# Kernel optimization log

Measured on AMD Instinct MI355X. Metric: run time of the kernel, lower is better.

## Reference

```python
import jax, jax.numpy as jnp
import numpy as np

B, T, C = 4, 2048, 1024
N_HEAD = 16
HEAD_DIM = C // N_HEAD


def setup_inputs() -> dict:
    key = jax.random.key(0)
    kx, kk, kq, kv, kp = jax.random.split(key, 5)
    s = 1.0 / np.sqrt(C)
    return {
        "x": jax.random.normal(kx, (B, T, C), dtype=jnp.float32),
        "Wk": jax.random.normal(kk, (C, C), dtype=jnp.float32) * s,
        "Wq": jax.random.normal(kq, (C, C), dtype=jnp.float32) * s,
        "Wv": jax.random.normal(kv, (C, C), dtype=jnp.float32) * s,
        "Wp": jax.random.normal(kp, (C, C), dtype=jnp.float32) * s,
    }


def reference(x, Wk, Wq, Wv, Wp):
    b, t, c = x.shape
    # torch nn.Linear(y = x @ W.T); split heads -> [B, H, T, D]
    def heads(w):
        return jnp.einsum("btc,ec->bte", x, w).reshape(b, t, N_HEAD, HEAD_DIM).transpose(0, 2, 1, 3)
    k = heads(Wk)
    q = heads(Wq)
    v = heads(Wv)
    scale = 1.0 / np.sqrt(HEAD_DIM).astype(np.float32)
    att = jnp.einsum("bhqd,bhkd->bhqk", q, k) * scale  # [B,H,T,T]
    causal = jnp.tril(jnp.ones((t, t), dtype=bool))
    att = jnp.where(causal[None, None], att, -jnp.inf)
    att = jax.nn.softmax(att, axis=-1)
    y = jnp.einsum("bhqk,bhkd->bhqd", att, v)  # [B,H,T,D]
    y = y.transpose(0, 2, 1, 3).reshape(b, t, c)
    return jnp.einsum("btc,ec->bte", y, Wp)
```

## Files before the change

### kernel.cpp

```cpp
#include <hip/hip_runtime.h>

typedef __bf16 bf16x8 __attribute__((ext_vector_type(8)));
typedef float f32x4 __attribute__((ext_vector_type(4)));
typedef float f32x16 __attribute__((ext_vector_type(16)));
typedef unsigned short u16x8 __attribute__((ext_vector_type(8)));
typedef unsigned short u16x4 __attribute__((ext_vector_type(4)));
typedef unsigned u32x4 __attribute__((ext_vector_type(4)));

#define BB 4
#define TT 2048
#define CC 1024
#define HH 16
#define DD 64

__device__ __forceinline__ unsigned short f2bf(float f){
  unsigned u = __builtin_bit_cast(unsigned, f);
  u += 0x7FFFu + ((u >> 16) & 1u);
  return (unsigned short)(u >> 16);
}
__device__ __forceinline__ bf16x8 as_bf(u16x8 v){ return __builtin_bit_cast(bf16x8, v); }
__device__ __forceinline__ unsigned cvt_pk(float lo, float hi){
  unsigned r; asm("v_cvt_pk_bf16_f32 %0, %1, %2" : "=v"(r) : "v"(lo), "v"(hi)); return r;
}
__device__ __forceinline__ void pl32swap(unsigned &a, unsigned &b){
  asm("v_permlane32_swap_b32 %0, %1" : "+v"(a), "+v"(b));
}
__device__ __forceinline__ float ex2(float x){
#if __has_builtin(__builtin_amdgcn_exp2f)
  return __builtin_amdgcn_exp2f(x);
#else
  return __expf(x * 0.6931471805599453f);
#endif
}

__global__ __launch_bounds__(256) void cvt_all(const float* __restrict__ x,
                                               const float* __restrict__ Wk,
                                               const float* __restrict__ Wq,
                                               const float* __restrict__ Wv,
                                               const float* __restrict__ Wp,
                                               unsigned short* __restrict__ xb,
                                               unsigned short* __restrict__ wb){
  const int i = blockIdx.x * 256 + threadIdx.x;
  constexpr int EX = (BB*TT*CC)/4;
  const float* src; unsigned short* dst; int off;
  if (i < EX){ src = x; dst = xb; off = i; }
  else {
    const int j = i - EX;
    const int wsel = j >> 18;
    off = j & 262143;
    src = (wsel==0) ? Wk : (wsel==1) ? Wq : (wsel==2) ? Wv : Wp;
    dst = wb + ((size_t)wsel << 20);
  }
  const float4 f = ((const float4*)src)[off];
  u16x4 o; o.x = f2bf(f.x); o.y = f2bf(f.y); o.z = f2bf(f.z); o.w = f2bf(f.w);
  ((u16x4*)dst)[off] = o;
}

template<int NX, bool QKV>
__global__ __launch_bounds__(256) void gemm128(const unsigned short* __restrict__ A,
                                               const unsigned short* __restrict__ Bm,
                                               void* __restrict__ o0, void* __restrict__ o1,
                                               void* __restrict__ o2){
  constexpr int K = 1024;
  constexpr int NWG = NX * 64;
  __shared__ __align__(16) unsigned short As[128*64];
  __shared__ __align__(16) unsigned short Bs[128*64];
  const int tid = threadIdx.x;
  const int flat = blockIdx.y * NX + blockIdx.x;
  const int swz = (flat & 7) * (NWG / 8) + (flat >> 3);
  const int n0 = (swz % NX) * 128;
  const int m0 = (swz / NX) * 128;
  const int w = tid >> 6, lane = tid & 63, l15 = lane & 15, g = lane >> 4;
  const int wm = (w >> 1) * 64, wn = (w & 1) * 64;

  f32x4 acc[4][4] = {};

  for (int k0 = 0; k0 < K; k0 += 64){
    #pragma unroll
    for (int i = 0; i < 4; ++i){
      const int p = i*256 + tid;
      const int r = p >> 3, c = p & 7;
      const int gc = c ^ (r & 7);
      __builtin_amdgcn_global_load_lds(
        (const __attribute__((address_space(1))) void*)(A + (size_t)(m0 + r)*K + k0 + gc*8),
        (__attribute__((address_space(3))) void*)(As + p*8), 16, 0, 0);
    }
    #pragma unroll
    for (int i = 0; i < 4; ++i){
      const int p = i*256 + tid;
      const int r = p >> 3, c = p & 7;
      const int gc = c ^ (r & 7);
      __builtin_amdgcn_global_load_lds(
        (const __attribute__((address_space(1))) void*)(Bm + (size_t)(n0 + r)*K + k0 + gc*8),
        (__attribute__((address_space(3))) void*)(Bs + p*8), 16, 0, 0);
    }
    __syncthreads();

    bf16x8 af[2][4], bfr[2][4];
    #pragma unroll
    for (int ks = 0; ks < 2; ++ks){
      #pragma unroll
      for (int m = 0; m < 4; ++m){
        const int R = wm + m*16 + l15;
        const int c = (ks*4 + g) ^ (R & 7);
        af[ks][m] = as_bf(*(const u16x8*)(As + R*64 + c*8));
      }
      #pragma unroll
      for (int n = 0; n < 4; ++n){
        const int R = wn + n*16 + l15;
        const int c = (ks*4 + g) ^ (R & 7);
        bfr[ks][n] = as_bf(*(const u16x8*)(Bs + R*64 + c*8));
      }
    }
    #pragma unroll
    for (int ks = 0; ks < 2; ++ks)
      #pragma unroll
      for (int m = 0; m < 4; ++m)
        #pragma unroll
        for (int n = 0; n < 4; ++n)
          acc[m][n] = __builtin_amdgcn_mfma_f32_16x16x32_bf16(af[ks][m], bfr[ks][n], acc[m][n], 0, 0, 0);
    __syncthreads();
  }

  const int tsel = n0 >> 10;
  const float sc = (QKV && tsel == 1) ? 0.18033688011112042f : 1.0f;
  unsigned short* outb = nullptr;
  if (QKV) outb = (unsigned short*)(tsel == 0 ? o0 : tsel == 1 ? o1 : o2);

  #pragma unroll
  for (int m = 0; m < 4; ++m)
    #pragma unroll
    for (int n = 0; n < 4; ++n)
      #pragma unroll
      for (int r = 0; r < 4; ++r){
        const int row = m0 + wm + m*16 + g*4 + r;
        const int col = n0 + wn + n*16 + l15;
        const float v = acc[m][n][r];
        if (QKV) outb[(size_t)row*1024 + (col & 1023)] = f2bf(v * sc);
        else     ((float*)o0)[(size_t)row*1024 + col] = v;
      }
}

__global__ __launch_bounds__(256) void transpose_v(const unsigned short* __restrict__ V,
                                                   unsigned short* __restrict__ Vt){
  __shared__ unsigned short Ts[64*72];
  const int kt = blockIdx.x, bh = blockIdx.y;
  const int b = bh >> 4, h = bh & 15;
  const int tid = threadIdx.x;
  #pragma unroll
  for (int i = 0; i < 2; ++i){
    const int p = i*256 + tid, r = p >> 3, c = p & 7;
    *(u16x8*)(Ts + r*72 + c*8) =
      *(const u16x8*)(V + (size_t)b*TT*CC + (size_t)(kt*64 + r)*CC + h*DD + c*8);
  }
  __syncthreads();
  #pragma unroll
  for (int i = 0; i < 2; ++i){
    const int p = i*256 + tid, d = p >> 3, c = p & 7;
    u16x8 v;
    #pragma unroll
    for (int j = 0; j < 8; ++j) v[j] = Ts[(c*8 + j)*72 + d];
    *(u16x8*)(Vt + ((size_t)bh*DD + d)*TT + (size_t)kt*64 + ((c ^ (d & 7))*8)) = v;
  }
}

__global__ __launch_bounds__(512, 4) void attn2(const unsigned short* __restrict__ Q,
                                                const unsigned short* __restrict__ Km,
                                                const unsigned short* __restrict__ Vt,
                                                unsigned short* __restrict__ Y){
  __shared__ __align__(16) unsigned short Ks[3][64*64];
  __shared__ __align__(16) unsigned short Vs[3][64*64];
  const int bh = blockIdx.x, b = bh >> 4, h = bh & 15;
  const int qt = 7 - blockIdx.y;
  const int tid = threadIdx.x;
  const int w = tid >> 6, lane = tid & 63, l31 = lane & 31, hi = lane >> 5;
  const int q0 = qt * 256;
  const int wq0 = q0 + w * 32;
  const int wqmax = wq0 + 31;
  const int nkt = 4 * qt + 4;
  const int qg = wq0 + l31;

  const unsigned short* Ksrc = Km + (size_t)b*TT*CC + h*DD;
  const unsigned short* Vsrc = Vt + (size_t)bh*DD*TT;

  auto stage = [&](int buf, int kt){
    const int r = tid >> 3, c = tid & 7;
    const int gc = c ^ (r & 7);
    __builtin_amdgcn_global_load_lds(
      (const __attribute__((address_space(1))) void*)(Ksrc + (size_t)(kt*64 + r)*CC + gc*8),
      (__attribute__((address_space(3))) void*)(&Ks[buf][tid*8]), 16, 0, 0);
    __builtin_amdgcn_global_load_lds(
      (const __attribute__((address_space(1))) void*)(Vsrc + (size_t)r*TT + (size_t)kt*64 + c*8),
      (__attribute__((address_space(3))) void*)(&Vs[buf][tid*8]), 16, 0, 0);
  };

  stage(0, 0);

  const unsigned short* qrow = Q + ((size_t)b*TT + wq0 + l31)*CC + h*DD;
  bf16x8 qf[4];
  #pragma unroll
  for (int ds = 0; ds < 4; ++ds)
    qf[ds] = as_bf(*(const u16x8*)(qrow + 16*ds + 8*hi));

  int koff[4];
  #pragma unroll
  for (int ds = 0; ds < 4; ++ds)
    koff[ds] = l31*64 + (((2*ds + hi) ^ (l31 & 7)) * 8);

  float m_ = -1e30f, l_ = 0.f;
  f32x16 y0 = {}, y1 = {};

  int cb = 0;
  for (int t = 0; t < nkt; ++t){
    const int nx = (cb == 2) ? 0 : cb + 1;
    if (t + 1 < nkt){
      stage(nx, t + 1);
      asm volatile("s_waitcnt vmcnt(2)" ::: "memory");
    } else {
      asm volatile("s_waitcnt vmcnt(0)" ::: "memory");
    }
    __builtin_amdgcn_s_barrier();

    if (t*64 <= wqmax){
      const unsigned short* Kp = &Ks[cb][0];
      const unsigned short* Vp = &Vs[cb][0];

      f32x16 s0 = {}, s1 = {};
      __builtin_amdgcn_s_setprio(1);
      #pragma unroll
      for (int ds = 0; ds < 4; ++ds){
        bf16x8 kf0 = as_bf(*(const u16x8*)(Kp + koff[ds]));
        s0 = __builtin_amdgcn_mfma_f32_32x32x16_bf16(kf0, qf[ds], s0, 0, 0, 0);
        bf16x8 kf1 = as_bf(*(const u16x8*)(Kp + koff[ds] + 2048));
        s1 = __builtin_amdgcn_mfma_f32_32x32x16_bf16(kf1, qf[ds], s1, 0, 0, 0);
      }
      __builtin_amdgcn_s_setprio(0);

      if (t*64 + 63 > wq0){
        const int kb0 = t*64;
        #pragma unroll
        for (int r = 0; r < 16; ++r){
          const int kr = (r & 3) + 8*(r >> 2) + 4*hi;
          if (kb0 + kr      > qg) s0[r] = -1e30f;
          if (kb0 + 32 + kr > qg) s1[r] = -1e30f;
        }
      }

      float tm[8];
      #pragma unroll
      for (int r = 0; r < 8; ++r) tm[r] = fmaxf(fmaxf(s0[r], s0[r+8]), fmaxf(s1[r], s1[r+8]));
      #pragma unroll
      for (int r = 0; r < 4; ++r) tm[r] = fmaxf(tm[r], tm[r+4]);
      float pmax = fmaxf(fmaxf(tm[0], tm[2]), fmaxf(tm[1], tm[3]));
      pmax = fmaxf(pmax, __shfl_xor(pmax, 32));

      if (!__all(pmax <= m_ + 8.f)){
        const float mnew = fmaxf(m_, pmax);
        const float alpha = ex2(m_ - mnew);
        l_ *= alpha;
        #pragma unroll
        for (int r = 0; r < 16; ++r){
          const float ar = __shfl(alpha, (r & 3) + 8*(r >> 2) + 4*hi);
          y0[r] *= ar; y1[r] *= ar;
        }
        m_ = mnew;
      }

      #pragma unroll
      for (int r = 0; r < 16; ++r) s0[r] = ex2(s0[r] - m_);
      #pragma unroll
      for (int r = 0; r < 16; ++r) s1[r] = ex2(s1[r] - m_);
      float ts[8];
      #pragma unroll
      for (int r = 0; r < 8; ++r) ts[r] = (s0[r] + s0[r+8]) + (s1[r] + s1[r+8]);
      #pragma unroll
      for (int r = 0; r < 4; ++r) ts[r] += ts[r+4];
      float rs = (ts[0] + ts[2]) + (ts[1] + ts[3]);
      rs += __shfl_xor(rs, 32);
      l_ += rs;

      __builtin_amdgcn_s_setprio(1);
      #pragma unroll
      for (int m = 0; m < 4; ++m){
        const f32x16 c = (m < 2) ? s0 : s1;
        const int bx = (m & 1) * 8;
        unsigned A0 = cvt_pk(c[bx+0], c[bx+1]);
        unsigned B0 = cvt_pk(c[bx+4], c[bx+5]);
        pl32swap(A0, B0);
        unsigned A1 = cvt_pk(c[bx+2], c[bx+3]);
        unsigned B1 = cvt_pk(c[bx+6], c[bx+7]);
        pl32swap(A1, B1);
        u32x4 pw; pw.x = A0; pw.y = A1; pw.z = B0; pw.w = B1;
        const bf16x8 pa = __builtin_bit_cast(bf16x8, pw);
        bf16x8 vf0 = as_bf(*(const u16x8*)(Vp + koff[m]));
        y0 = __builtin_amdgcn_mfma_f32_32x32x16_bf16(pa, vf0, y0, 0, 0, 0);
        bf16x8 vf1 = as_bf(*(const u16x8*)(Vp + koff[m] + 2048));
        y1 = __builtin_amdgcn_mfma_f32_32x32x16_bf16(pa, vf1, y1, 0, 0, 0);
      }
      __builtin_amdgcn_s_setprio(0);
    }
    cb = nx;
  }

  const float linv = 1.f / l_;
  #pragma unroll
  for (int r = 0; r < 16; ++r){
    const int qlr = (r & 3) + 8*(r >> 2) + 4*hi;
    const float lr = __shfl(linv, qlr);
    unsigned short* yp = Y + ((size_t)b*TT + wq0 + qlr)*CC + h*DD + l31;
    yp[0]  = f2bf(y0[r] * lr);
    yp[32] = f2bf(y1[r] * lr);
  }
}

extern "C" void kernel_launch(void* const* d_in, const int* in_sizes, int n_in,
                              void* d_out, int out_size, void* d_ws, size_t ws_size,
                              hipStream_t stream){
  const float* x  = (const float*)d_in[0];
  const float* Wk = (const float*)d_in[1];
  const float* Wq = (const float*)d_in[2];
  const float* Wv = (const float*)d_in[3];
  const float* Wp = (const float*)d_in[4];

  const size_t E  = (size_t)BB*TT*CC;
  const size_t Wn = (size_t)CC*CC;
  unsigned short* ws  = (unsigned short*)d_ws;
  unsigned short* xb  = ws;
  unsigned short* wkb = xb  + E;
  unsigned short* wqb = wkb + Wn;
  unsigned short* wvb = wqb + Wn;
  unsigned short* wpb = wvb + Wn;
  unsigned short* qb  = wpb + Wn;
  unsigned short* kb  = qb  + E;
  unsigned short* vb  = kb  + E;
  unsigned short* vt  = vb  + E;

  cvt_all<<<12288, 256, 0, stream>>>(x, Wk, Wq, Wv, Wp, xb, wkb);

  gemm128<24, true><<<dim3(24, 64), 256, 0, stream>>>(xb, wkb, kb, qb, vb);

  transpose_v<<<dim3(TT/64, BB*HH), 256, 0, stream>>>(vb, vt);

  unsigned short* yb = xb;
  attn2<<<dim3(BB*HH, TT/256), 512, 0, stream>>>(qb, kb, vt, yb);

  gemm128<8, false><<<dim3(8, 64), 256, 0, stream>>>(yb, wpb, (float*)d_out, nullptr, nullptr);
}
```

Baseline: 164.2 us.

## Fuse V transpose into QKV GEMM epilogue and reorder attention q-tiles

For V output tiles, the QKV GEMM now computes the transposed product by swapping the MFMA operands, then writes straight into the swizzled per-head V-transposed layout. This removes the separate transpose_v kernel and its global round trip. The attention grid's q-tile order also changes from strictly descending to heavy-first then light tiles, which alters load balance. In exchange, the V epilogue does scattered 2-byte stores, which may coalesce poorly.

```diff
diff --git a/kernel.cpp b/kernel.cpp
--- a/kernel.cpp
+++ b/kernel.cpp
@@ -72,6 +72,7 @@
   const int m0 = (swz / NX) * 128;
   const int w = tid >> 6, lane = tid & 63, l15 = lane & 15, g = lane >> 4;
   const int wm = (w >> 1) * 64, wn = (w & 1) * 64;
+  const int tsel = QKV ? (n0 >> 10) : 0;
 
   f32x4 acc[4][4] = {};
 
@@ -112,20 +113,50 @@
         bfr[ks][n] = as_bf(*(const u16x8*)(Bs + R*64 + c*8));
       }
     }
-    #pragma unroll
-    for (int ks = 0; ks < 2; ++ks)
+    if (!QKV || tsel != 2){
+      #pragma unroll
+      for (int ks = 0; ks < 2; ++ks)
+        #pragma unroll
+        for (int m = 0; m < 4; ++m)
+          #pragma unroll
+          for (int n = 0; n < 4; ++n)
+            acc[m][n] = __builtin_amdgcn_mfma_f32_16x16x32_bf16(af[ks][m], bfr[ks][n], acc[m][n], 0, 0, 0);
+    } else {
+      #pragma unroll
+      for (int ks = 0; ks < 2; ++ks)
+        #pragma unroll
+        for (int n = 0; n < 4; ++n)
+          #pragma unroll
+          for (int m = 0; m < 4; ++m)
+            acc[n][m] = __builtin_amdgcn_mfma_f32_16x16x32_bf16(bfr[ks][n], af[ks][m], acc[n][m], 0, 0, 0);
+    }
+    __syncthreads();
+  }
+
+  if (QKV && tsel == 2){
+    const int bq = m0 >> 11;
+    const int t0 = m0 & 2047;
+    unsigned short* vt = (unsigned short*)o2;
+    #pragma unroll
+    for (int n = 0; n < 4; ++n)
       #pragma unroll
       for (int m = 0; m < 4; ++m)
         #pragma unroll
-        for (int n = 0; n < 4; ++n)
-          acc[m][n] = __builtin_amdgcn_mfma_f32_16x16x32_bf16(af[ks][m], bfr[ks][n], acc[m][n], 0, 0, 0);
-    __syncthreads();
-  }
-
-  const int tsel = n0 >> 10;
+        for (int r = 0; r < 4; ++r){
+          const int cg = (n0 & 1023) + wn + n*16 + g*4 + r;
+          const int h = cg >> 6, d = cg & 63;
+          const int t = t0 + wm + m*16 + l15;
+          const int kt = t >> 6, cch = (t >> 3) & 7, j = t & 7;
+          const size_t idx = ((size_t)(bq*HH + h)*DD + d)*TT
+                           + (size_t)kt*64 + ((cch ^ (d & 7)) << 3) + j;
+          vt[idx] = f2bf(acc[n][m][r]);
+        }
+    return;
+  }
+
   const float sc = (QKV && tsel == 1) ? 0.18033688011112042f : 1.0f;
   unsigned short* outb = nullptr;
-  if (QKV) outb = (unsigned short*)(tsel == 0 ? o0 : tsel == 1 ? o1 : o2);
+  if (QKV) outb = (unsigned short*)(tsel == 0 ? o0 : o1);
 
   #pragma unroll
   for (int m = 0; m < 4; ++m)
@@ -139,29 +170,6 @@
         if (QKV) outb[(size_t)row*1024 + (col & 1023)] = f2bf(v * sc);
         else     ((float*)o0)[(size_t)row*1024 + col] = v;
       }
-}
-
-__global__ __launch_bounds__(256) void transpose_v(const unsigned short* __restrict__ V,
-                                                   unsigned short* __restrict__ Vt){
-  __shared__ unsigned short Ts[64*72];
-  const int kt = blockIdx.x, bh = blockIdx.y;
-  const int b = bh >> 4, h = bh & 15;
-  const int tid = threadIdx.x;
-  #pragma unroll
-  for (int i = 0; i < 2; ++i){
-    const int p = i*256 + tid, r = p >> 3, c = p & 7;
-    *(u16x8*)(Ts + r*72 + c*8) =
-      *(const u16x8*)(V + (size_t)b*TT*CC + (size_t)(kt*64 + r)*CC + h*DD + c*8);
-  }
-  __syncthreads();
-  #pragma unroll
-  for (int i = 0; i < 2; ++i){
-    const int p = i*256 + tid, d = p >> 3, c = p & 7;
-    u16x8 v;
-    #pragma unroll
-    for (int j = 0; j < 8; ++j) v[j] = Ts[(c*8 + j)*72 + d];
-    *(u16x8*)(Vt + ((size_t)bh*DD + d)*TT + (size_t)kt*64 + ((c ^ (d & 7))*8)) = v;
-  }
 }
 
 __global__ __launch_bounds__(512, 4) void attn2(const unsigned short* __restrict__ Q,
@@ -171,7 +179,8 @@
   __shared__ __align__(16) unsigned short Ks[3][64*64];
   __shared__ __align__(16) unsigned short Vs[3][64*64];
   const int bh = blockIdx.x, b = bh >> 4, h = bh & 15;
-  const int qt = 7 - blockIdx.y;
+  const int yq = blockIdx.y;
+  const int qt = (yq < 4) ? (7 - yq) : (yq - 4);
   const int tid = threadIdx.x;
   const int w = tid >> 6, lane = tid & 63, l31 = lane & 31, hi = lane >> 5;
   const int q0 = qt * 256;
@@ -332,14 +341,11 @@
   unsigned short* wpb = wvb + Wn;
   unsigned short* qb  = wpb + Wn;
   unsigned short* kb  = qb  + E;
-  unsigned short* vb  = kb  + E;
-  unsigned short* vt  = vb  + E;
+  unsigned short* vt  = kb  + E;
 
   cvt_all<<<12288, 256, 0, stream>>>(x, Wk, Wq, Wv, Wp, xb, wkb);
 
-  gemm128<24, true><<<dim3(24, 64), 256, 0, stream>>>(xb, wkb, kb, qb, vb);
-
-  transpose_v<<<dim3(TT/64, BB*HH), 256, 0, stream>>>(vb, vt);
+  gemm128<24, true><<<dim3(24, 64), 256, 0, stream>>>(xb, wkb, kb, qb, vt);
 
   unsigned short* yb = xb;
   attn2<<<dim3(BB*HH, TT/256), 512, 0, stream>>>(qb, kb, vt, yb);
```

Result: faster. 159.2 us (-3.0%).
